# Performance work log

Hardware: AMD Instinct MI355X
Metric: run time of the kernel (lower is better)

## Reference

```python
import jax, jax.numpy as jnp
import numpy as np


def setup_inputs() -> dict:
    key = jax.random.key(0)
    k1, k2, k3, k4 = jax.random.split(key, 4)
    B, A, C = 16, 65536, 21  # batch, anchors, num_classes+1 (20 fg classes + background)
    loc_preds = jax.random.normal(k1, (B, A, 4), dtype=jnp.float32)
    loc_targets = jax.random.normal(k2, (B, A, 4), dtype=jnp.float32)
    cls_preds = jax.random.normal(k3, (B, A, C), dtype=jnp.float32)
    # -1 = ignore, 0 = background/negative, 1..20 = positive classes
    cls_targets = jax.random.randint(k4, (B, A), -1, C)
    pos = cls_targets > 0
    return {
        "loc_preds": loc_preds,
        "loc_targets": loc_targets,
        "cls_preds": cls_preds,
        "cls_targets": cls_targets,
        "pos": pos,
        "verbose": 0,
    }


def reference(loc_preds, loc_targets, cls_preds, cls_targets, pos, verbose):
    eps = 1e-7
    num_pos = jnp.sum(pos).astype(loc_preds.dtype)

    # smooth L1 over positive anchors (sum reduction, beta=1), mask instead of gather
    posf = pos[..., None].astype(loc_preds.dtype)          # [B, A, 1]
    d = loc_preds - loc_targets
    ad = jnp.abs(d)
    sl1 = jnp.where(ad < 1.0, 0.5 * d * d, ad - 0.5)
    loc_loss = jnp.sum(sl1 * posf)

    # focal loss over non-ignored anchors (cls_targets > -1)
    pos_neg = (cls_targets > -1)[..., None].astype(cls_preds.dtype)  # [B, A, 1]
    C = cls_preds.shape[-1]
    y = jax.nn.one_hot(cls_targets, C, dtype=cls_preds.dtype)  # -1 -> all zeros
    p = jax.nn.softmax(cls_preds, axis=-1)
    p = jnp.clip(p, eps, 1.0 - eps)
    fl = -y * jnp.log(p) * (1.0 - p) ** 2
    cls_loss = jnp.sum(fl * pos_neg)

    return (loc_loss + cls_loss) / num_pos
```

## Files before the change

kernel.cpp:

```cpp
#include <hip/hip_runtime.h>

#define NCLS 21
#define BLK 256
#define APT 2
#define SPAN (BLK * APT)

__device__ __forceinline__ float4 load_f4u(const float* p) {
    float4 v; __builtin_memcpy(&v, p, 16); return v;
}

__device__ __forceinline__ float fmax4(const float4& v) {
    return fmaxf(fmaxf(v.x, v.y), fmaxf(v.z, v.w));
}
__device__ __forceinline__ float4 fmax44(const float4& a, const float4& b) {
    return make_float4(fmaxf(a.x, b.x), fmaxf(a.y, b.y),
                       fmaxf(a.z, b.z), fmaxf(a.w, b.w));
}

__device__ __forceinline__ float focal_regs(
    int t, const float4& c0, const float4& c1, const float4& c2,
    const float4& c3, const float4& c4, float c20)
{
    float m = fmaxf(fmax4(fmax44(fmax44(c0, c1), fmax44(c2, c3))),
                    fmaxf(fmax4(c4), c20));
    float s = 0.0f, et = 0.0f;
#define FSTEP(val, idx) { float e = __expf((val) - m); s += e; et = (t == (idx)) ? e : et; }
    FSTEP(c0.x, 0)  FSTEP(c0.y, 1)  FSTEP(c0.z, 2)  FSTEP(c0.w, 3)
    FSTEP(c1.x, 4)  FSTEP(c1.y, 5)  FSTEP(c1.z, 6)  FSTEP(c1.w, 7)
    FSTEP(c2.x, 8)  FSTEP(c2.y, 9)  FSTEP(c2.z, 10) FSTEP(c2.w, 11)
    FSTEP(c3.x, 12) FSTEP(c3.y, 13) FSTEP(c3.z, 14) FSTEP(c3.w, 15)
    FSTEP(c4.x, 16) FSTEP(c4.y, 17) FSTEP(c4.z, 18) FSTEP(c4.w, 19)
    FSTEP(c20,  20)
#undef FSTEP
    float pt = et / s;
    pt = fminf(fmaxf(pt, 1e-7f), 1.0f - 1e-7f);
    float om = 1.0f - pt;
    return -__logf(pt) * om * om;
}

__device__ __forceinline__ float smooth_l1(const float4& lp, const float4& lt) {
    float d0 = lp.x - lt.x, d1 = lp.y - lt.y, d2 = lp.z - lt.z, d3 = lp.w - lt.w;
    float a0 = fabsf(d0), a1 = fabsf(d1), a2 = fabsf(d2), a3 = fabsf(d3);
    float s = 0.0f;
    s += (a0 < 1.0f) ? 0.5f * d0 * d0 : a0 - 0.5f;
    s += (a1 < 1.0f) ? 0.5f * d1 * d1 : a1 - 0.5f;
    s += (a2 < 1.0f) ? 0.5f * d2 * d2 : a2 - 0.5f;
    s += (a3 < 1.0f) ? 0.5f * d3 * d3 : a3 - 0.5f;
    return s;
}

__global__ __launch_bounds__(BLK) void focal_main(
    const float* __restrict__ loc_p,
    const float* __restrict__ loc_t,
    const float* __restrict__ cls_p,
    const int*   __restrict__ cls_t,
    float2* __restrict__ partials,
    int n_anchors)
{
    __shared__ float redL[4], redP[4];

    const int tid  = threadIdx.x;
    const int wave = tid >> 6;
    const int lane = tid & 63;
    const long long a0 = (long long)blockIdx.x * SPAN + tid;
    const long long a1 = a0 + BLK;

    float acc = 0.0f, npos = 0.0f;
    const bool v0 = (a0 < n_anchors), v1 = (a1 < n_anchors);

    int t0 = -1, t1 = -1;
    float4 lp0, lt0, lp1, lt1;
    float4 c00, c01, c02, c03, c04; float c0_20 = 0.0f;
    float4 c10, c11, c12, c13, c14; float c1_20 = 0.0f;

    if (v0) {
        t0  = cls_t[a0];
        lp0 = ((const float4*)loc_p)[a0];
        lt0 = ((const float4*)loc_t)[a0];
        const float* g = cls_p + a0 * NCLS;
        c00 = load_f4u(g);      c01 = load_f4u(g + 4);  c02 = load_f4u(g + 8);
        c03 = load_f4u(g + 12); c04 = load_f4u(g + 16); c0_20 = g[20];
    }
    if (v1) {
        t1  = cls_t[a1];
        lp1 = ((const float4*)loc_p)[a1];
        lt1 = ((const float4*)loc_t)[a1];
        const float* g = cls_p + a1 * NCLS;
        c10 = load_f4u(g);      c11 = load_f4u(g + 4);  c12 = load_f4u(g + 8);
        c13 = load_f4u(g + 12); c14 = load_f4u(g + 16); c1_20 = g[20];
    }

    if (v0) {
        if (t0 > 0)  { acc += smooth_l1(lp0, lt0); npos += 1.0f; }
        if (t0 >= 0) acc += focal_regs(t0, c00, c01, c02, c03, c04, c0_20);
    }
    if (v1) {
        if (t1 > 0)  { acc += smooth_l1(lp1, lt1); npos += 1.0f; }
        if (t1 >= 0) acc += focal_regs(t1, c10, c11, c12, c13, c14, c1_20);
    }

    #pragma unroll
    for (int off = 32; off > 0; off >>= 1) {
        acc  += __shfl_down(acc,  off, 64);
        npos += __shfl_down(npos, off, 64);
    }
    if (lane == 0) { redL[wave] = acc; redP[wave] = npos; }
    __syncthreads();
    if (tid == 0)
        partials[blockIdx.x] = make_float2(redL[0] + redL[1] + redL[2] + redL[3],
                                           redP[0] + redP[1] + redP[2] + redP[3]);
}

#define RBLK 1024
__global__ __launch_bounds__(RBLK) void focal_reduce(
    const float2* __restrict__ partials, float* __restrict__ out, int npart)
{
    __shared__ float red[32];
    float L = 0.0f, P = 0.0f;
    for (int i = threadIdx.x; i < npart; i += RBLK) {
        float2 v = partials[i];
        L += v.x; P += v.y;
    }
    #pragma unroll
    for (int off = 32; off > 0; off >>= 1) {
        L += __shfl_down(L, off, 64);
        P += __shfl_down(P, off, 64);
    }
    const int wave = threadIdx.x >> 6, lane = threadIdx.x & 63;
    if (lane == 0) { red[wave * 2] = L; red[wave * 2 + 1] = P; }
    __syncthreads();
    if (threadIdx.x == 0) {
        float Ls = 0.0f, Ps = 0.0f;
        #pragma unroll
        for (int w = 0; w < RBLK / 64; ++w) { Ls += red[w * 2]; Ps += red[w * 2 + 1]; }
        out[0] = Ls / Ps;
    }
}

extern "C" void kernel_launch(void* const* d_in, const int* in_sizes, int n_in,
                              void* d_out, int out_size, void* d_ws, size_t ws_size,
                              hipStream_t stream)
{
    const float* loc_p = (const float*)d_in[0];
    const float* loc_t = (const float*)d_in[1];
    const float* cls_p = (const float*)d_in[2];
    const int*   cls_t = (const int*)d_in[3];
    float*  out = (float*)d_out;
    float2* ws  = (float2*)d_ws;

    const int n_anchors = in_sizes[3];
    const int blocks = (n_anchors + SPAN - 1) / SPAN;

    focal_main<<<blocks, BLK, 0, stream>>>(loc_p, loc_t, cls_p, cls_t, ws, n_anchors);
    focal_reduce<<<1, RBLK, 0, stream>>>(ws, out, blocks);
}
```

Before: 165.1 us.

## Stage class logits tile into LDS via direct global-to-LDS loads

Replaces the per-thread strided, unaligned 84-byte loads of class logits with a cooperative, fully coalesced copy of the block's contiguous logit tile into shared memory using global_load_lds, then reads each anchor's row from LDS. The goal is to avoid poorly coalesced global accesses. In exchange it uses about 43KB of LDS per block, which cuts occupancy, and adds a barrier plus LDS reads whose stride of 21 may cause bank conflicts.

After: 167.8 us. About the same (+1.6%).

```diff
diff --git a/kernel.cpp b/kernel.cpp
--- a/kernel.cpp
+++ b/kernel.cpp
@@ -1,13 +1,16 @@
 #include <hip/hip_runtime.h>
+#include <stdint.h>
 
 #define NCLS 21
 #define BLK 256
 #define APT 2
 #define SPAN (BLK * APT)
+#define CLS_ROW_BYTES (NCLS * 4)
+#define CLS_TILE_BYTES (SPAN * CLS_ROW_BYTES)
+#define NCHUNK (CLS_TILE_BYTES / 1024)
 
-__device__ __forceinline__ float4 load_f4u(const float* p) {
-    float4 v; __builtin_memcpy(&v, p, 16); return v;
-}
+typedef __attribute__((address_space(3))) void       lds_void_t;
+typedef __attribute__((address_space(1))) const void gbl_void_t;
 
 __device__ __forceinline__ float fmax4(const float4& v) {
     return fmaxf(fmaxf(v.x, v.y), fmaxf(v.z, v.w));
@@ -38,6 +41,17 @@
     return -__logf(pt) * om * om;
 }
 
+__device__ __forceinline__ float focal_lds(int t, const float* __restrict__ row)
+{
+    float4 c0  = make_float4(row[0],  row[1],  row[2],  row[3]);
+    float4 c1  = make_float4(row[4],  row[5],  row[6],  row[7]);
+    float4 c2  = make_float4(row[8],  row[9],  row[10], row[11]);
+    float4 c3  = make_float4(row[12], row[13], row[14], row[15]);
+    float4 c4  = make_float4(row[16], row[17], row[18], row[19]);
+    float  c20 = row[20];
+    return focal_regs(t, c0, c1, c2, c3, c4, c20);
+}
+
 __device__ __forceinline__ float smooth_l1(const float4& lp, const float4& lt) {
     float d0 = lp.x - lt.x, d1 = lp.y - lt.y, d2 = lp.z - lt.z, d3 = lp.w - lt.w;
     float a0 = fabsf(d0), a1 = fabsf(d1), a2 = fabsf(d2), a3 = fabsf(d3);
@@ -57,46 +71,61 @@
     float2* __restrict__ partials,
     int n_anchors)
 {
+    __shared__ float cls_s[SPAN * NCLS];
     __shared__ float redL[4], redP[4];
 
     const int tid  = threadIdx.x;
     const int wave = tid >> 6;
     const int lane = tid & 63;
-    const long long a0 = (long long)blockIdx.x * SPAN + tid;
+    const long long blk0       = (long long)blockIdx.x * SPAN;
+    const long long base_byte  = blk0 * CLS_ROW_BYTES;
+    const long long total_byte = (long long)n_anchors * CLS_ROW_BYTES;
+
+    {
+        const char* g = (const char*)cls_p + base_byte + (long long)lane * 16;
+        char*       l = (char*)cls_s;
+        for (int c = wave; c < NCHUNK; c += BLK / 64) {
+            const long long gb = base_byte + (long long)c * 1024 + lane * 16;
+            if (gb + 16 <= total_byte) {
+                __builtin_amdgcn_global_load_lds(
+                    (gbl_void_t*)(g + (long long)c * 1024),
+                    (lds_void_t*)(l + c * 1024),
+                    16, 0, 0);
+            } else if (gb < total_byte) {
+                for (long long b = gb; b < total_byte; b += 4)
+                    cls_s[(b - base_byte) >> 2] = cls_p[b >> 2];
+            }
+        }
+    }
+
+    const long long a0 = blk0 + tid;
     const long long a1 = a0 + BLK;
-
-    float acc = 0.0f, npos = 0.0f;
     const bool v0 = (a0 < n_anchors), v1 = (a1 < n_anchors);
 
     int t0 = -1, t1 = -1;
     float4 lp0, lt0, lp1, lt1;
-    float4 c00, c01, c02, c03, c04; float c0_20 = 0.0f;
-    float4 c10, c11, c12, c13, c14; float c1_20 = 0.0f;
-
     if (v0) {
         t0  = cls_t[a0];
         lp0 = ((const float4*)loc_p)[a0];
         lt0 = ((const float4*)loc_t)[a0];
-        const float* g = cls_p + a0 * NCLS;
-        c00 = load_f4u(g);      c01 = load_f4u(g + 4);  c02 = load_f4u(g + 8);
-        c03 = load_f4u(g + 12); c04 = load_f4u(g + 16); c0_20 = g[20];
     }
     if (v1) {
         t1  = cls_t[a1];
         lp1 = ((const float4*)loc_p)[a1];
         lt1 = ((const float4*)loc_t)[a1];
-        const float* g = cls_p + a1 * NCLS;
-        c10 = load_f4u(g);      c11 = load_f4u(g + 4);  c12 = load_f4u(g + 8);
-        c13 = load_f4u(g + 12); c14 = load_f4u(g + 16); c1_20 = g[20];
     }
 
+    asm volatile("s_waitcnt vmcnt(0)" ::: "memory");
+    __syncthreads();
+
+    float acc = 0.0f, npos = 0.0f;
     if (v0) {
         if (t0 > 0)  { acc += smooth_l1(lp0, lt0); npos += 1.0f; }
-        if (t0 >= 0) acc += focal_regs(t0, c00, c01, c02, c03, c04, c0_20);
+        if (t0 >= 0) acc += focal_lds(t0, cls_s + tid * NCLS);
     }
     if (v1) {
         if (t1 > 0)  { acc += smooth_l1(lp1, lt1); npos += 1.0f; }
-        if (t1 >= 0) acc += focal_regs(t1, c10, c11, c12, c13, c14, c1_20);
+        if (t1 >= 0) acc += focal_lds(t1, cls_s + (tid + BLK) * NCLS);
     }
 
     #pragma unroll
```
